# Optimization experiments

Hardware: AMD Instinct MI355X
Metric: run time of the kernel (lower is better)

The kernel has to match this reference:

```python
import jax, jax.numpy as jnp
import numpy as np

B, T, D, K = 16, 4096, 512, 256
ALPHA_MIN = 1e-6


def setup_inputs() -> dict:
    key = jax.random.key(0)
    ks = jax.random.split(key, 5)
    x = jax.random.normal(ks[0], (B, T, D), dtype=jnp.float32)
    # s_imag ~ U(-pi, pi) as in reset_parameters
    s_imag = jax.random.uniform(ks[1], (K,), minval=-np.pi, maxval=np.pi, dtype=jnp.float32)
    # s_real_raw = softplus^{-1}(target_alpha - alpha_min), target_alpha ~ U(0.01, 0.2)
    target_alpha = jax.random.uniform(ks[2], (K,), minval=0.01, maxval=0.2, dtype=jnp.float32)
    y = jnp.clip(target_alpha - ALPHA_MIN, 1e-8, None)
    s_real_raw = jnp.log(jnp.expm1(y))
    # projection weight/bias (spectral norm applied inside reference)
    W = jax.random.normal(ks[3], (K, D), dtype=jnp.float32) / np.sqrt(D)
    b = jnp.zeros((K,), dtype=jnp.float32)
    tau_raw = jnp.zeros((), dtype=jnp.float32)
    return {"x": x, "s_real_raw": s_real_raw, "s_imag": s_imag,
            "tau_raw": tau_raw, "W": W, "b": b}


def _spectral_normalize(W):
    # one power iteration from a fixed random u (mirrors torch spectral_norm buffer,
    # n_power_iterations=1, eps=1e-7); u,v are stop-gradiented like torch buffers.
    eps = 1e-7
    u0 = jax.random.normal(jax.random.key(42), (W.shape[0],), dtype=W.dtype)
    u0 = u0 / jnp.maximum(jnp.linalg.norm(u0), eps)
    v = W.T @ u0
    v = v / jnp.maximum(jnp.linalg.norm(v), eps)
    u = W @ v
    u = u / jnp.maximum(jnp.linalg.norm(u), eps)
    u = jax.lax.stop_gradient(u)
    v = jax.lax.stop_gradient(v)
    sigma = u @ (W @ v)
    return W / sigma


def reference(x, s_real_raw, s_imag, tau_raw, W, b):
    Bx, Tx, Dx = x.shape
    k = s_imag.shape[0]
    tau = jax.nn.softplus(tau_raw) + 1e-3
    alpha0 = (jax.nn.softplus(s_real_raw) + ALPHA_MIN) * tau  # [k]
    omega0 = s_imag * tau                                     # [k]
    # dt is None path: uniform normalized time step
    dt = jnp.asarray(1.0 / max(Tx - 1, 1), dtype=x.dtype)
    rho = jnp.exp(-alpha0 * dt)   # [k], time-invariant since dt is constant
    ct = jnp.cos(omega0 * dt)     # [k]
    st = jnp.sin(omega0 * dt)     # [k]
    # spectral-normalized linear drive u_t = W_sn x_t + b  -> [B,T,k]
    u = jnp.einsum('btd,kd->btk', x, _spectral_normalize(W)) + b

    def step(carry, u_t):
        c, s = carry  # each [B,k]
        c_new = rho * (c * ct - s * st) + u_t
        s_new = rho * (c * st + s * ct)
        return (c_new, s_new), (c_new, s_new)

    z0 = (jnp.zeros((Bx, k), x.dtype), jnp.zeros((Bx, k), x.dtype))
    _, (C, S) = jax.lax.scan(step, z0, jnp.swapaxes(u, 0, 1))  # [T,B,k] each
    C = jnp.swapaxes(C, 0, 1)
    S = jnp.swapaxes(S, 0, 1)
    return jnp.concatenate([C, S], axis=2)  # [B,T,2k]
```

## Files before the change

kernel.cpp:

```cpp
#include <hip/hip_runtime.h>

#define Bsz 16
#define Tsz 4096
#define Dsz 512
#define Ksz 256
#define Msz (Bsz * Tsz)
#define CHUNK 64
#define NCH (Tsz / CHUNK)

typedef __attribute__((ext_vector_type(8))) short short8;
typedef __attribute__((ext_vector_type(4))) float f32x4;

__device__ __forceinline__ unsigned int rotl32(unsigned int x, int d) {
  return (x << d) | (x >> (32 - d));
}

__device__ void threefry_pair(unsigned int c0, unsigned int c1,
                              unsigned int& o0, unsigned int& o1) {
  const unsigned int k0 = 0u, k1 = 42u;
  const unsigned int k2 = k0 ^ k1 ^ 0x1BD11BDAu;
  unsigned int x0 = c0 + k0;
  unsigned int x1 = c1 + k1;
#define TF_ROUND(r) { x0 += x1; x1 = rotl32(x1, (r)); x1 ^= x0; }
  TF_ROUND(13) TF_ROUND(15) TF_ROUND(26) TF_ROUND(6)
  x0 += k1; x1 += k2 + 1u;
  TF_ROUND(17) TF_ROUND(29) TF_ROUND(16) TF_ROUND(24)
  x0 += k2; x1 += k0 + 2u;
  TF_ROUND(13) TF_ROUND(15) TF_ROUND(26) TF_ROUND(6)
  x0 += k0; x1 += k1 + 3u;
  TF_ROUND(17) TF_ROUND(29) TF_ROUND(16) TF_ROUND(24)
  x0 += k1; x1 += k2 + 4u;
  TF_ROUND(13) TF_ROUND(15) TF_ROUND(26) TF_ROUND(6)
  x0 += k2; x1 += k0 + 5u;
#undef TF_ROUND
  o0 = x0; o1 = x1;
}

__device__ float erfinv32(float x) {
  float w = -log1pf(-x * x);
  float p;
  if (w < 5.f) {
    w -= 2.5f;
    p = 2.81022636e-08f;
    p = fmaf(p, w, 3.43273939e-07f);
    p = fmaf(p, w, -3.5233877e-06f);
    p = fmaf(p, w, -4.39150654e-06f);
    p = fmaf(p, w, 0.00021858087f);
    p = fmaf(p, w, -0.00125372503f);
    p = fmaf(p, w, -0.00417768164f);
    p = fmaf(p, w, 0.246640727f);
    p = fmaf(p, w, 1.50140941f);
  } else {
    w = sqrtf(w) - 3.f;
    p = -0.000200214257f;
    p = fmaf(p, w, 0.000100950558f);
    p = fmaf(p, w, 0.00134934322f);
    p = fmaf(p, w, -0.00367342844f);
    p = fmaf(p, w, 0.00573950773f);
    p = fmaf(p, w, -0.0076224613f);
    p = fmaf(p, w, 0.00943887047f);
    p = fmaf(p, w, 1.00167406f);
    p = fmaf(p, w, 2.83297682f);
  }
  return p * x;
}

__device__ float bits_to_normal(unsigned int bits) {
  unsigned int fb = (bits >> 9) | 0x3f800000u;
  float f = __uint_as_float(fb) - 1.0f;
  const float lo = -0.99999994f;
  float u = f * 2.0f + lo;
  u = fmaxf(lo, u);
  return 1.41421356f * erfinv32(u);
}

__device__ float block_sum_512(float v, float* s_red) {
  #pragma unroll
  for (int o = 32; o > 0; o >>= 1) v += __shfl_down(v, o);
  const int lane = threadIdx.x & 63, wid = threadIdx.x >> 6;
  if (lane == 0) s_red[wid] = v;
  __syncthreads();
  float r = 0.f;
  #pragma unroll
  for (int i = 0; i < 8; ++i) r += s_red[i];
  __syncthreads();
  return r;
}

__device__ __forceinline__ unsigned int bf16rne(float f) {
  unsigned int u = __float_as_uint(f);
  return (u + 0x7FFFu + ((u >> 16) & 1u)) >> 16;
}

__device__ __forceinline__ void split2(float v0, float v1,
                                       unsigned int& hh, unsigned int& ll) {
  unsigned int u0 = __float_as_uint(v0);
  unsigned int u1 = __float_as_uint(v1);
  hh = __builtin_amdgcn_perm(u1, u0, 0x07060302u);
  float r0 = v0 - __uint_as_float(u0 & 0xFFFF0000u);
  float r1 = v1 - __uint_as_float(u1 & 0xFFFF0000u);
  unsigned int r;
  asm("v_cvt_pk_bf16_f32 %0, %1, %2" : "=v"(r) : "v"(r0), "v"(r1));
  ll = r;
}

__global__ __launch_bounds__(512) void prep1_kernel(
    const float* __restrict__ W, float* __restrict__ partial_v) {
  __shared__ float s_u0[Ksz];
  __shared__ float s_red[8];
  const int tid = threadIdx.x;
  if (tid < 128) {
    unsigned int y0, y1;
    threefry_pair((unsigned int)tid, (unsigned int)(tid + 128), y0, y1);
    s_u0[tid] = bits_to_normal(y0);
    s_u0[tid + 128] = bits_to_normal(y1);
  }
  __syncthreads();
  float val = (tid < Ksz) ? s_u0[tid] * s_u0[tid] : 0.f;
  float ss = block_sum_512(val, s_red);
  float inv = 1.f / fmaxf(sqrtf(ss), 1e-7f);

  const int k0 = blockIdx.x * 16;
  float acc = 0.f;
  #pragma unroll
  for (int kk = 0; kk < 16; ++kk)
    acc = fmaf(W[(size_t)(k0 + kk) * Dsz + tid], s_u0[k0 + kk], acc);
  partial_v[blockIdx.x * Dsz + tid] = acc * inv;
}

__global__ __launch_bounds__(512) void prep2_kernel(
    const float* __restrict__ W, const float* __restrict__ partial_v,
    float* __restrict__ wv) {
  __shared__ float s_v[Dsz];
  __shared__ float s_red[8];
  __shared__ float s_p[8];
  const int tid = threadIdx.x;
  float acc = 0.f;
  #pragma unroll
  for (int b = 0; b < 16; ++b) acc += partial_v[b * Dsz + tid];
  float ssv = block_sum_512(acc * acc, s_red);
  float invv = 1.f / fmaxf(sqrtf(ssv), 1e-7f);
  s_v[tid] = acc * invv;
  __syncthreads();

  const int k = blockIdx.x * 4 + (tid >> 7);
  const int sub = tid & 127;
  const float* wr = W + (size_t)k * Dsz;
  float p = 0.f;
  #pragma unroll
  for (int j = sub; j < Dsz; j += 128) p = fmaf(wr[j], s_v[j], p);
  #pragma unroll
  for (int o = 32; o > 0; o >>= 1) p += __shfl_down(p, o);
  const int lane = tid & 63, wid = tid >> 6;
  if (lane == 0) s_p[wid] = p;
  __syncthreads();
  if (tid < 4) wv[blockIdx.x * 4 + tid] = s_p[2 * tid] + s_p[2 * tid + 1];
}

__global__ __launch_bounds__(256) void prep3_kernel(
    const float* __restrict__ s_real_raw, const float* __restrict__ s_imag,
    const float* __restrict__ tau_raw, const float* __restrict__ wv,
    float* __restrict__ consts) {
  __shared__ float s_p[4];
  const int tid = threadIdx.x;
  float v = wv[tid];
  float v2 = v * v;
  #pragma unroll
  for (int o = 32; o > 0; o >>= 1) v2 += __shfl_down(v2, o);
  const int lane = tid & 63, wid = tid >> 6;
  if (lane == 0) s_p[wid] = v2;
  __syncthreads();
  float sswv = s_p[0] + s_p[1] + s_p[2] + s_p[3];
  float sigma = sswv / fmaxf(sqrtf(sswv), 1e-7f);
  if (tid == 0) consts[12 * Ksz] = 1.f / sigma;

  float tr = tau_raw[0];
  float tau = fmaxf(tr, 0.f) + log1pf(expf(-fabsf(tr))) + 1e-3f;
  float srr = s_real_raw[tid];
  float sp = fmaxf(srr, 0.f) + log1pf(expf(-fabsf(srr)));
  float alpha0 = (sp + 1e-6f) * tau;
  float omega0 = s_imag[tid] * tau;
  const float dt = 1.f / 4095.f;
  float ad = alpha0 * dt, an = omega0 * dt;
  consts[tid]            = expf(-ad) * cosf(an);
  consts[Ksz + tid]      = expf(-ad) * sinf(an);
  consts[2 * Ksz + tid]  = expf(-ad * 64.f) * cosf(an * 64.f);
  consts[3 * Ksz + tid]  = expf(-ad * 64.f) * sinf(an * 64.f);
  consts[4 * Ksz + tid]  = expf(-ad * 4.f) * cosf(an * 4.f);
  consts[5 * Ksz + tid]  = expf(-ad * 4.f) * sinf(an * 4.f);
  consts[6 * Ksz + tid]  = expf(-ad * 8.f) * cosf(an * 8.f);
  consts[7 * Ksz + tid]  = expf(-ad * 8.f) * sinf(an * 8.f);
  consts[8 * Ksz + tid]  = expf(-ad * 16.f) * cosf(an * 16.f);
  consts[9 * Ksz + tid]  = expf(-ad * 16.f) * sinf(an * 16.f);
  consts[10 * Ksz + tid] = expf(-ad * 32.f) * cosf(an * 32.f);
  consts[11 * Ksz + tid] = expf(-ad * 32.f) * sinf(an * 32.f);
}

__global__ __launch_bounds__(64) void wpack_kernel(
    const float* __restrict__ W, const float* __restrict__ consts,
    unsigned int* __restrict__ WfH, unsigned int* __restrict__ WfL) {
  const int kb = blockIdx.x >> 4;
  const int nb = blockIdx.x & 15;
  const int lane = threadIdx.x;
  const int lr = lane & 15, lg = lane >> 4;
  const float inv_sigma = consts[12 * Ksz];
  const float* src = W + (size_t)(nb * 16 + lr) * Dsz + kb * 32 + lg * 8;
  float v[8];
  *(float4*)&v[0] = *(const float4*)src;
  *(float4*)&v[4] = *(const float4*)(src + 4);
  unsigned int hh[4], ll[4];
  #pragma unroll
  for (int i = 0; i < 4; ++i)
    split2(v[2 * i] * inv_sigma, v[2 * i + 1] * inv_sigma, hh[i], ll[i]);
  const size_t off = (size_t)blockIdx.x * 256 + lane * 4;
  *(int4*)(WfH + off) = *(int4*)hh;
  *(int4*)(WfL + off) = *(int4*)ll;
}

__global__ __launch_bounds__(512, 2) void gemm_mfma(
    const float* __restrict__ X, const unsigned int* __restrict__ WfH,
    const unsigned int* __restrict__ WfL, const float* __restrict__ bias,
    const float* __restrict__ consts, unsigned short* __restrict__ U,
    float* __restrict__ carry) {
  __shared__ unsigned int ldsA[2][4096];

  const int tid = threadIdx.x;
  const size_t m0 = (size_t)blockIdx.x * 128;

  const int sr = tid >> 2;
  const int sc = (tid & 3) * 8;
  const float* gx = X + (m0 + sr) * Dsz + sc;
  const int swz = (sr & 7) << 4;
  const int aoff_h = sr * 128 + ((sc * 2) ^ swz);
  const int aoff_l = sr * 128 + ((64 + sc * 2) ^ swz);

  const int lane = tid & 63;
  const int wid = tid >> 6;
  const int wm = wid >> 2;
  const int wn = wid & 3;
  const int lr = lane & 15;
  const int lg = lane >> 4;

  float xaA[8], xaB[8];
  #define LOAD_A(dst, kb) do {                             \
    const float* p = gx + (kb) * 32;                       \
    *(float4*)&dst[0] = *(const float4*)p;                 \
    *(float4*)&dst[4] = *(const float4*)(p + 4);           \
  } while (0)

  const char* const wfh = (const char*)WfH + (size_t)wn * 4096 + lane * 16;
  const char* const wfl = (const char*)WfL + (size_t)wn * 4096 + lane * 16;

  short8 bhA[4], blA[4], bhB[4], blB[4];
  #define LOAD_B(bh_, bl_, kb) do {                                          \
    const size_t tb = (size_t)(kb) * 16384;                                  \
    _Pragma("unroll")                                                        \
    for (int f = 0; f < 4; ++f) {                                            \
      bh_[f] = *(const short8*)(wfh + tb + (size_t)f * 1024);                \
      bl_[f] = *(const short8*)(wfl + tb + (size_t)f * 1024);                \
    }                                                                        \
  } while (0)

  #define CONVERT_STORE(xa, buf) do {                                        \
    char* const Ab_ = (char*)ldsA[(buf)];                                    \
    unsigned int hh[4], llw[4];                                              \
    _Pragma("unroll")                                                        \
    for (int i = 0; i < 4; ++i)                                              \
      split2(xa[2 * i], xa[2 * i + 1], hh[i], llw[i]);                       \
    *(int4*)(Ab_ + aoff_h) = *(int4*)hh;                                     \
    *(int4*)(Ab_ + aoff_l) = *(int4*)llw;                                    \
  } while (0)

  short8 ah[4], al[4];
  #define DS_READ(buf) do {                                                  \
    const char* const Ab_ = (const char*)ldsA[(buf)];                        \
    _Pragma("unroll")                                                        \
    for (int f = 0; f < 4; ++f) {                                            \
      const int r = wm * 64 + f * 16 + lr;                                   \
      const int sz = (r & 7) << 4;                                           \
      ah[f] = *(const short8*)(Ab_ + r * 128 + ((lg * 16) ^ sz));            \
      al[f] = *(const short8*)(Ab_ + r * 128 + ((64 + lg * 16) ^ sz));       \
    }                                                                        \
  } while (0)

  f32x4 acc[4][4];
  #pragma unroll
  for (int i = 0; i < 4; ++i)
    #pragma unroll
    for (int j = 0; j < 4; ++j) acc[i][j] = (f32x4)(0.f);

  #define MFMA48(bh_, bl_) do {                                              \
    _Pragma("unroll")                                                        \
    for (int mf = 0; mf < 4; ++mf)                                           \
      _Pragma("unroll")                                                      \
      for (int nf = 0; nf < 4; ++nf)                                         \
        acc[mf][nf] = __builtin_amdgcn_mfma_f32_16x16x32_bf16(               \
            ah[mf], bh_[nf], acc[mf][nf], 0, 0, 0);                          \
    _Pragma("unroll")                                                        \
    for (int mf = 0; mf < 4; ++mf)                                           \
      _Pragma("unroll")                                                      \
      for (int nf = 0; nf < 4; ++nf)                                         \
        acc[mf][nf] = __builtin_amdgcn_mfma_f32_16x16x32_bf16(               \
            ah[mf], bl_[nf], acc[mf][nf], 0, 0, 0);                          \
    _Pragma("unroll")                                                        \
    for (int mf = 0; mf < 4; ++mf)                                           \
      _Pragma("unroll")                                                      \
      for (int nf = 0; nf < 4; ++nf)                                         \
        acc[mf][nf] = __builtin_amdgcn_mfma_f32_16x16x32_bf16(               \
            al[mf], bh_[nf], acc[mf][nf], 0, 0, 0);                          \
  } while (0)

  #define SYNC() do {                                                        \
    asm volatile("s_waitcnt lgkmcnt(0)" ::: "memory");                       \
    __builtin_amdgcn_s_barrier();                                            \
    __builtin_amdgcn_sched_barrier(0);                                       \
  } while (0)

  LOAD_A(xaA, 0);
  LOAD_A(xaB, 1);
  LOAD_B(bhA, blA, 0);

  #define BODY(kb, xa, bhC, blC, bhN, blN) do {                              \
    if ((kb) + 1 < 16) LOAD_B(bhN, blN, (kb) + 1);        \
    CONVERT_STORE(xa, (kb) & 1);                                             \
    if ((kb) + 2 < 16) LOAD_A(xa, (kb) + 2);                   \
    SYNC();                                                                  \
    DS_READ((kb) & 1);                                                       \
    MFMA48(bhC, blC);                                                        \
  } while (0)

  for (int kb = 0; kb < 16; kb += 2) {
    BODY(kb,     xaA, bhA, blA, bhB, blB);
    BODY(kb + 1, xaB, bhB, blB, bhA, blA);
  }
  #undef BODY
  #undef SYNC
  #undef MFMA48
  #undef DS_READ
  #undef CONVERT_STORE
  #undef LOAD_B
  #undef LOAD_A

  #pragma unroll
  for (int nf = 0; nf < 4; ++nf) {
    const int n = wn * 64 + nf * 16 + lr;
    const float bv = bias[n];
    const float ar_ = consts[n],           ai_ = consts[Ksz + n];
    const float p4r = consts[4 * Ksz + n], p4i = consts[5 * Ksz + n];
    const float p8r = consts[6 * Ksz + n], p8i = consts[7 * Ksz + n];
    const float p16r = consts[8 * Ksz + n], p16i = consts[9 * Ksz + n];
    const int e = 3 - lg;
    const float b1r = (e & 1) ? p4r : 1.f, b1i = (e & 1) ? p4i : 0.f;
    const float b2r = (e & 2) ? p8r : 1.f, b2i = (e & 2) ? p8i : 0.f;
    float wr = b1r * b2r - b1i * b2i;
    float wi = b1r * b2i + b1i * b2r;
    float Sr = 0.f, Si = 0.f;
    #pragma unroll
    for (int mf = 3; mf >= 0; --mf) {
      float vr = wr, vi = wi;
      #pragma unroll
      for (int j = 3; j >= 0; --j) {
        const float u = acc[mf][nf][j] + bv;
        U[(m0 + wm * 64 + mf * 16 + lg * 4 + j) * Ksz + n] =
            (unsigned short)bf16rne(u);
        Sr = fmaf(u, vr, Sr);
        Si = fmaf(u, vi, Si);
        if (j) {
          float t_ = vr * ar_ - vi * ai_;
          vi = vr * ai_ + vi * ar_;
          vr = t_;
        }
      }
      if (mf) {
        float t_ = wr * p16r - wi * p16i;
        wi = wr * p16i + wi * p16r;
        wr = t_;
      }
    }
    Sr += __shfl_xor(Sr, 16); Si += __shfl_xor(Si, 16);
    Sr += __shfl_xor(Sr, 32); Si += __shfl_xor(Si, 32);
    if (lg == 0)
      ((float2*)carry)[(size_t)(blockIdx.x * 2 + wm) * Ksz + n] =
          make_float2(Sr, Si);
  }
}

__global__ __launch_bounds__(64) void scan_prefix(
    const float* __restrict__ consts, const float* __restrict__ carry,
    float* __restrict__ prefix) {
  const int k = blockIdx.y * 64 + threadIdx.x;
  const int b = blockIdx.x;
  const float Ar = consts[2 * Ksz + k], Ai = consts[3 * Ksz + k];
  const float2* cp = (const float2*)carry;
  float2* pp = (float2*)prefix;
  float c = 0.f, s = 0.f;
  for (int m = 0; m < NCH; ++m) {
    const size_t idx = (size_t)(b * NCH + m) * Ksz + k;
    pp[idx] = make_float2(c, s);
    float2 L = cp[idx];
    float cn = fmaf(Ar, c, fmaf(-Ai, s, L.x));
    float sn = fmaf(Ai, c, fmaf(Ar, s, L.y));
    c = cn; s = sn;
  }
}

__global__ __launch_bounds__(256) void scan_final(
    const unsigned short* __restrict__ U, const float* __restrict__ consts,
    const float* __restrict__ prefix, float* __restrict__ out) {
  const int tid = threadIdx.x;
  const int bm = blockIdx.x * 4 + (tid >> 6);
  const int k0 = (tid & 63) * 4;
  float ar[4], ai[4], c[4], s[4];
  #pragma unroll
  for (int j = 0; j < 4; ++j) {
    ar[j] = consts[k0 + j];
    ai[j] = consts[Ksz + k0 + j];
    float2 w = ((const float2*)prefix)[(size_t)bm * Ksz + k0 + j];
    c[j] = w.x; s[j] = w.y;
  }
  const unsigned short* up = U + (size_t)bm * (CHUNK * Ksz) + k0;
  float* op = out + (size_t)bm * (CHUNK * 2 * Ksz) + k0;
  for (int t = 0; t < CHUNK; ++t) {
    unsigned long long uv = *(const unsigned long long*)(up + (size_t)t * Ksz);
    #pragma unroll
    for (int j = 0; j < 4; ++j) {
      float u = __uint_as_float(((unsigned int)(uv >> (16 * j))) << 16);
      float cn = fmaf(ar[j], c[j], fmaf(-ai[j], s[j], u));
      s[j] = fmaf(ai[j], c[j], ar[j] * s[j]);
      c[j] = cn;
    }
    *(float4*)(op + (size_t)t * 2 * Ksz) = make_float4(c[0], c[1], c[2], c[3]);
    *(float4*)(op + (size_t)t * 2 * Ksz + Ksz) =
        make_float4(s[0], s[1], s[2], s[3]);
  }
}

extern "C" void kernel_launch(void* const* d_in, const int* in_sizes, int n_in,
                              void* d_out, int out_size, void* d_ws, size_t ws_size,
                              hipStream_t stream) {
  const float* x    = (const float*)d_in[0];
  const float* srr  = (const float*)d_in[1];
  const float* sim  = (const float*)d_in[2];
  const float* traw = (const float*)d_in[3];
  const float* W    = (const float*)d_in[4];
  const float* bias = (const float*)d_in[5];
  float* out = (float*)d_out;

  float* wsf    = (float*)d_ws;
  float* consts = wsf;
  unsigned short* U = (unsigned short*)(wsf + 4096);
  float* carry  = wsf + 4096 + 8388608;
  float* prefix = carry + (size_t)2 * Bsz * NCH * Ksz;
  unsigned int* WfH = (unsigned int*)(prefix + (size_t)2 * Bsz * NCH * Ksz);
  unsigned int* WfL = WfH + 65536;
  float* partial_v  = (float*)(WfL + 65536);
  float* wv         = partial_v + 16 * Dsz;

  prep1_kernel<<<16, 512, 0, stream>>>(W, partial_v);
  prep2_kernel<<<64, 512, 0, stream>>>(W, partial_v, wv);
  prep3_kernel<<<1, 256, 0, stream>>>(srr, sim, traw, wv, consts);
  wpack_kernel<<<256, 64, 0, stream>>>(W, consts, WfH, WfL);
  gemm_mfma<<<Msz / 128, 512, 0, stream>>>(x, WfH, WfL, bias, consts, U, carry);
  scan_prefix<<<dim3(Bsz, Ksz / 64), 64, 0, stream>>>(consts, carry, prefix);
  scan_final<<<Bsz * NCH / 4, 256, 0, stream>>>(U, consts, prefix, out);
}
```

Measured before the change: 113.9 us.

## Process two K-blocks per barrier in GEMM and prefetch carries in scan prefix

The GEMM main loop now stores two K-blocks of converted A into a 4-slot LDS buffer, then does a single barrier before running MFMAs for both blocks. This halves the number of barriers per tile. In exchange, LDS use doubles to 64KB per block, which may limit occupancy at 2 blocks per CU, and the B loads for each pair are issued together. Separately, the scan_prefix loop loads the next chunk's carry one iteration early so the global load latency overlaps the serial recurrence.

Result: no change. 112.6 us (-1.1%).

```diff
diff --git a/kernel.cpp b/kernel.cpp
--- a/kernel.cpp
+++ b/kernel.cpp
@@ -222,7 +222,7 @@
     const unsigned int* __restrict__ WfL, const float* __restrict__ bias,
     const float* __restrict__ consts, unsigned short* __restrict__ U,
     float* __restrict__ carry) {
-  __shared__ unsigned int ldsA[2][4096];
+  __shared__ unsigned int ldsA[4][4096];
 
   const int tid = threadIdx.x;
   const size_t m0 = (size_t)blockIdx.x * 128;
@@ -318,22 +318,26 @@
 
   LOAD_A(xaA, 0);
   LOAD_A(xaB, 1);
-  LOAD_B(bhA, blA, 0);
-
-  #define BODY(kb, xa, bhC, blC, bhN, blN) do {                              \
-    if ((kb) + 1 < 16) LOAD_B(bhN, blN, (kb) + 1);        \
-    CONVERT_STORE(xa, (kb) & 1);                                             \
-    if ((kb) + 2 < 16) LOAD_A(xa, (kb) + 2);                   \
+
+  #define PHASE(k0, p) do {                                                  \
+    LOAD_B(bhA, blA, (k0));                                                  \
+    LOAD_B(bhB, blB, (k0) + 1);                                              \
+    CONVERT_STORE(xaA, (p));                                                 \
+    if ((k0) + 2 < 16) LOAD_A(xaA, (k0) + 2);                                \
+    CONVERT_STORE(xaB, (p) + 1);                                             \
+    if ((k0) + 3 < 16) LOAD_A(xaB, (k0) + 3);                                \
     SYNC();                                                                  \
-    DS_READ((kb) & 1);                                                       \
-    MFMA48(bhC, blC);                                                        \
-  } while (0)
-
-  for (int kb = 0; kb < 16; kb += 2) {
-    BODY(kb,     xaA, bhA, blA, bhB, blB);
-    BODY(kb + 1, xaB, bhB, blB, bhA, blA);
-  }
-  #undef BODY
+    DS_READ(p);                                                              \
+    MFMA48(bhA, blA);                                                        \
+    DS_READ((p) + 1);                                                        \
+    MFMA48(bhB, blB);                                                        \
+  } while (0)
+
+  for (int s = 0; s < 8; s += 2) {
+    PHASE(2 * s, 0);
+    PHASE(2 * s + 2, 2);
+  }
+  #undef PHASE
   #undef SYNC
   #undef MFMA48
   #undef DS_READ
@@ -393,14 +397,17 @@
   const float Ar = consts[2 * Ksz + k], Ai = consts[3 * Ksz + k];
   const float2* cp = (const float2*)carry;
   float2* pp = (float2*)prefix;
+  const size_t base = (size_t)(b * NCH) * Ksz + k;
   float c = 0.f, s = 0.f;
+  float2 L = cp[base];
   for (int m = 0; m < NCH; ++m) {
-    const size_t idx = (size_t)(b * NCH + m) * Ksz + k;
-    pp[idx] = make_float2(c, s);
-    float2 L = cp[idx];
+    float2 Lnext = make_float2(0.f, 0.f);
+    if (m + 1 < NCH) Lnext = cp[base + (size_t)(m + 1) * Ksz];
+    pp[base + (size_t)m * Ksz] = make_float2(c, s);
     float cn = fmaf(Ar, c, fmaf(-Ai, s, L.x));
     float sn = fmaf(Ai, c, fmaf(Ar, s, L.y));
     c = cn; s = sn;
+    L = Lnext;
   }
 }
 
```
